# Performance work log

Hardware: AMD Instinct MI355X
Metric: run time of the kernel (lower is better)

## Reference

```python
import jax, jax.numpy as jnp
import numpy as np

EPS = 1e-5
NH = 4          # num_heads
DH = 128        # head_dim
ALPHA = 1.0 / float(np.sqrt(DH))


def _ln(x, w, b):
    m = x.mean(-1, keepdims=True)
    v = x.var(-1, keepdims=True)
    return (x - m) * jax.lax.rsqrt(v + EPS) * w + b


def setup_inputs() -> dict:
    key = jax.random.key(0)
    ks = jax.random.split(key, 8)
    D = 512                 # hidden_size
    U = 4 * NH * DH         # uvqk linear out = 2048
    B, S, H = 32, 256, 2048  # batch, new tokens/seq, history len/seq
    NT = B * S              # 8192 flattened jagged tokens
    layer_input = jax.random.normal(ks[0], (NT, D), dtype=jnp.float32)
    hist_k = jax.random.normal(ks[1], (B, H, NH, DH), dtype=jnp.float32) * 0.1
    hist_v = jax.random.normal(ks[2], (B, H, NH, DH), dtype=jnp.float32) * 0.1
    # torch init: uniform(-0.5, 0.5); scaled down for numerical sanity
    W_uvqk = (jax.random.uniform(ks[3], (D, U), dtype=jnp.float32) - 0.5) * 0.1
    b_uvqk = (jax.random.uniform(ks[4], (U,), dtype=jnp.float32) - 0.5) * 0.1
    ln_in_w = jnp.ones((D,), jnp.float32)
    ln_in_b = jnp.zeros((D,), jnp.float32)
    ln_out_w = jnp.ones((NH * DH,), jnp.float32)
    ln_out_b = jnp.zeros((NH * DH,), jnp.float32)
    W_proj = jax.random.normal(ks[5], (NH * DH, D), dtype=jnp.float32) * 0.05
    return {
        "layer_input": layer_input, "hist_k": hist_k, "hist_v": hist_v,
        "ln_in_w": ln_in_w, "ln_in_b": ln_in_b,
        "W_uvqk": W_uvqk, "b_uvqk": b_uvqk,
        "ln_out_w": ln_out_w, "ln_out_b": ln_out_b, "W_proj": W_proj,
    }


def reference(layer_input, hist_k, hist_v, ln_in_w, ln_in_b,
              W_uvqk, b_uvqk, ln_out_w, ln_out_b, W_proj):
    B, H, nh, dh = hist_k.shape
    NT, D = layer_input.shape
    S = NT // B
    dspl = nh * dh
    # ln -> linear+bias -> silu (fused u,v,q,k projection)
    x = _ln(layer_input, ln_in_w, ln_in_b)
    uvqk = jax.nn.silu(x @ W_uvqk + b_uvqk)
    u, v, q, k = jnp.split(uvqk, 4, axis=-1)   # order: user, value, query, key
    q = q.reshape(B, S, nh, dh)
    k = k.reshape(B, S, nh, dh)
    v = v.reshape(B, S, nh, dh)
    # paged KV-cache append == concat new k,v after history
    K = jnp.concatenate([hist_k, k], axis=1)   # [B, T, nh, dh], T = H+S
    V = jnp.concatenate([hist_v, v], axis=1)
    T = H + S
    # HSTU varlen attention: silu(alpha * q k^T) with causal delta-q mask,
    # query i sits at global position H+i and may attend to kv pos <= H+i
    scores = jnp.einsum('bsnd,btnd->bnst', q, K) * ALPHA
    mask = jnp.arange(T)[None, :] <= (H + jnp.arange(S))[:, None]  # [S, T]
    p = jnp.where(mask[None, None], jax.nn.silu(scores), 0.0)
    attn = jnp.einsum('bnst,btnd->bsnd', p, V).reshape(NT, dspl)
    # gated output LN, projection, residual
    parallel = u * _ln(attn, ln_out_w, ln_out_b)
    return parallel @ W_proj + layer_input
```

## Files before the change

kernel.cpp:

```cpp
#include <hip/hip_runtime.h>
#include <hip/hip_bf16.h>


typedef __attribute__((ext_vector_type(8))) short v8s;
typedef __attribute__((ext_vector_type(4))) float v4f;
typedef __attribute__((ext_vector_type(16))) float v16f;
typedef __attribute__((ext_vector_type(4))) unsigned short v4us;
typedef __attribute__((ext_vector_type(4))) unsigned int v4u;

#define D_HID 512
#define U_DIM 2048
#define NHEAD 4
#define DHEAD 128
#define BATCH 32
#define SEQ   256
#define HIST  2048
#define NTOK  8192
#define ALPHA_ 0.08838834764831845f
#define EPS_   1e-5f

__device__ __forceinline__ unsigned short f2bf(float f) {
  unsigned int u = __float_as_uint(f);
  u += 0x7FFFu + ((u >> 16) & 1u);
  return (unsigned short)(u >> 16);
}
__device__ __forceinline__ float bf2f(unsigned short s) {
  return __uint_as_float(((unsigned int)s) << 16);
}
__device__ __forceinline__ float siluf(float x) {
  return x * __builtin_amdgcn_rcpf(1.0f + __expf(-x));
}
__device__ __forceinline__ unsigned int cvtpk(float lo, float hi) {
  __hip_bfloat162 h = __float22bfloat162_rn(make_float2(lo, hi));
  union { __hip_bfloat162 h; unsigned int u; } cv; cv.h = h;
  return cv.u;
}

__global__ __launch_bounds__(256) void ln_in_kernel(
    const float* __restrict__ x, const float* __restrict__ w,
    const float* __restrict__ b, unsigned short* __restrict__ out)
{
  int wid = threadIdx.x >> 6, lane = threadIdx.x & 63;
  int row = blockIdx.x * 4 + wid;
  const float* xr = x + (size_t)row * D_HID + lane * 8;
  float4 a0 = *(const float4*)xr;
  float4 a1 = *(const float4*)(xr + 4);
  float v[8] = {a0.x, a0.y, a0.z, a0.w, a1.x, a1.y, a1.z, a1.w};
  float s = 0.f, s2 = 0.f;
#pragma unroll
  for (int j = 0; j < 8; ++j) { s += v[j]; s2 += v[j] * v[j]; }
#pragma unroll
  for (int m = 1; m < 64; m <<= 1) { s += __shfl_xor(s, m, 64); s2 += __shfl_xor(s2, m, 64); }
  float mean = s * (1.f / D_HID);
  float var  = s2 * (1.f / D_HID) - mean * mean;
  float rstd = rsqrtf(var + EPS_);
  const float* wp = w + lane * 8; const float* bp = b + lane * 8;
  float4 w0 = *(const float4*)wp, w1 = *(const float4*)(wp + 4);
  float4 b0 = *(const float4*)bp, b1 = *(const float4*)(bp + 4);
  float wv[8] = {w0.x, w0.y, w0.z, w0.w, w1.x, w1.y, w1.z, w1.w};
  float bv[8] = {b0.x, b0.y, b0.z, b0.w, b1.x, b1.y, b1.z, b1.w};
  v8s o;
#pragma unroll
  for (int j = 0; j < 8; ++j) o[j] = (short)f2bf((v[j] - mean) * rstd * wv[j] + bv[j]);
  *(v8s*)(out + (size_t)row * D_HID + lane * 8) = o;
}

__global__ __launch_bounds__(256) void gated_ln_kernel(
    const float* __restrict__ attn0, const float* __restrict__ attn1,
    const unsigned short* __restrict__ uvqk,
    const float* __restrict__ w, const float* __restrict__ b,
    unsigned short* __restrict__ par)
{
  int wid = threadIdx.x >> 6, lane = threadIdx.x & 63;
  int row = blockIdx.x * 4 + wid;
  size_t off = (size_t)row * D_HID + lane * 8;
  float4 x0 = *(const float4*)(attn0 + off), x1 = *(const float4*)(attn0 + off + 4);
  float4 y0 = *(const float4*)(attn1 + off), y1 = *(const float4*)(attn1 + off + 4);
  float v[8] = {x0.x + y0.x, x0.y + y0.y, x0.z + y0.z, x0.w + y0.w,
                x1.x + y1.x, x1.y + y1.y, x1.z + y1.z, x1.w + y1.w};
  float s = 0.f, s2 = 0.f;
#pragma unroll
  for (int j = 0; j < 8; ++j) { s += v[j]; s2 += v[j] * v[j]; }
#pragma unroll
  for (int m = 1; m < 64; m <<= 1) { s += __shfl_xor(s, m, 64); s2 += __shfl_xor(s2, m, 64); }
  float mean = s * (1.f / D_HID);
  float var  = s2 * (1.f / D_HID) - mean * mean;
  float rstd = rsqrtf(var + EPS_);
  const float* wp = w + lane * 8; const float* bp = b + lane * 8;
  float4 w0 = *(const float4*)wp, w1 = *(const float4*)(wp + 4);
  float4 b0 = *(const float4*)bp, b1 = *(const float4*)(bp + 4);
  float wv[8] = {w0.x, w0.y, w0.z, w0.w, w1.x, w1.y, w1.z, w1.w};
  float bv[8] = {b0.x, b0.y, b0.z, b0.w, b1.x, b1.y, b1.z, b1.w};
  v8s uv = *(const v8s*)(uvqk + (size_t)row * U_DIM + lane * 8);
  v8s o;
#pragma unroll
  for (int j = 0; j < 8; ++j) {
    float u = bf2f((unsigned short)uv[j]);
    o[j] = (short)f2bf(u * ((v[j] - mean) * rstd * wv[j] + bv[j]));
  }
  *(v8s*)(par + (size_t)row * D_HID + lane * 8) = o;
}

__global__ __launch_bounds__(256) void transpose_w_kernel(
    const float* __restrict__ in, unsigned short* __restrict__ out, int R, int C)
{
  __shared__ float tile[32][33];
  int c0 = blockIdx.x * 32, r0 = blockIdx.y * 32;
  int tr = threadIdx.x >> 3;
  int tc = (threadIdx.x & 7) * 4;
  float4 vv = *(const float4*)(in + (size_t)(r0 + tr) * C + c0 + tc);
  tile[tr][tc + 0] = vv.x; tile[tr][tc + 1] = vv.y;
  tile[tr][tc + 2] = vv.z; tile[tr][tc + 3] = vv.w;
  __syncthreads();
  v4us o;
#pragma unroll
  for (int j = 0; j < 4; ++j) o[j] = f2bf(tile[tc + j][tr]);
  *(v4us*)(out + (size_t)(c0 + tr) * R + r0 + tc) = o;
}

template <int EPI>
__global__ __launch_bounds__(256) void gemm_kernel(
    const unsigned short* __restrict__ A, const unsigned short* __restrict__ Bt,
    int K, int N,
    const float* __restrict__ bias, const float* __restrict__ resid,
    unsigned short* __restrict__ outb, float* __restrict__ outf)
{
  __shared__ unsigned short Al[128 * 64];
  __shared__ unsigned short Bl[128 * 64];
  int m0 = blockIdx.x * 128, n0 = blockIdx.y * 128;
  int tid = threadIdx.x, lane = tid & 63, wid = tid >> 6;
  int wr = wid >> 1, wc = wid & 1;
  int lr = lane & 15, lg = lane >> 4;
  int rkey = (lr & 7) << 3;

  v4f acc[4][4];
#pragma unroll
  for (int i = 0; i < 4; ++i)
#pragma unroll
    for (int j = 0; j < 4; ++j) acc[i][j] = (v4f){0.f, 0.f, 0.f, 0.f};

  int srow = tid >> 3;
  int scol = ((tid & 7) * 8) ^ ((srow & 7) << 3);
  const unsigned short* gA = A  + (size_t)(m0 + srow) * K + scol;
  const unsigned short* gB = Bt + (size_t)(n0 + srow) * K + scol;

  for (int k0 = 0; k0 < K; k0 += 64) {
#pragma unroll
    for (int c = 0; c < 4; ++c) {
      __builtin_amdgcn_global_load_lds(
          (const __attribute__((address_space(1))) unsigned int*)(gA + (size_t)(c * 32) * K + k0),
          (__attribute__((address_space(3))) unsigned int*)&Al[c * 2048 + wid * 512], 16, 0, 0);
      __builtin_amdgcn_global_load_lds(
          (const __attribute__((address_space(1))) unsigned int*)(gB + (size_t)(c * 32) * K + k0),
          (__attribute__((address_space(3))) unsigned int*)&Bl[c * 2048 + wid * 512], 16, 0, 0);
    }
    asm volatile("s_waitcnt vmcnt(0)" ::: "memory");
    __syncthreads();
#pragma unroll
    for (int kk = 0; kk < 2; ++kk) {
      v8s af[4], bf[4];
#pragma unroll
      for (int mt = 0; mt < 4; ++mt)
        af[mt] = *(const v8s*)&Al[(wr * 64 + mt * 16 + lr) * 64 + ((kk * 32 + lg * 8) ^ rkey)];
#pragma unroll
      for (int nt = 0; nt < 4; ++nt)
        bf[nt] = *(const v8s*)&Bl[(wc * 64 + nt * 16 + lr) * 64 + ((kk * 32 + lg * 8) ^ rkey)];
#pragma unroll
      for (int mt = 0; mt < 4; ++mt)
#pragma unroll
        for (int nt = 0; nt < 4; ++nt)
          acc[mt][nt] = __builtin_amdgcn_mfma_f32_16x16x32_bf16(af[mt], bf[nt], acc[mt][nt], 0, 0, 0);
    }
    __syncthreads();
  }

#pragma unroll
  for (int nt = 0; nt < 4; ++nt) {
    int col = n0 + wc * 64 + nt * 16 + lr;
    float bi = 0.f;
    if constexpr (EPI == 0) bi = bias[col];
#pragma unroll
    for (int mt = 0; mt < 4; ++mt) {
      int row0 = m0 + wr * 64 + mt * 16 + lg * 4;
#pragma unroll
      for (int r = 0; r < 4; ++r) {
        float xv = acc[mt][nt][r];
        if constexpr (EPI == 0) {
          float rv = siluf(xv + bi);
          if ((unsigned)(col - 2 * D_HID) < (unsigned)D_HID) rv *= ALPHA_;
          outb[(size_t)(row0 + r) * N + col] = f2bf(rv);
        } else {
          outf[(size_t)(row0 + r) * N + col] = xv + resid[(size_t)(row0 + r) * N + col];
        }
      }
    }
  }
}

__global__ __launch_bounds__(512, 2) void attn_kernel(
    const float* __restrict__ histK, const float* __restrict__ histV,
    const unsigned short* __restrict__ uvqk, float* __restrict__ attn_out)
{
  __shared__ __align__(16) unsigned short Kl[2 * 64 * 128];
  __shared__ __align__(16) unsigned short Vt[2 * 128 * 64];

  int bid = blockIdx.x;
  int q   = bid >> 7;
  int b   = (bid >> 2) & 31;
  int n   = bid & 3;
  int tbase0 = q * 1152;
  const int NT = 18;

  int tid = threadIdx.x, lane = tid & 63, w = tid >> 6;
  int l5 = lane & 31;
  int hi = lane >> 5;
  int hi8 = hi * 8;
  int sq = w * 32 + l5;

  v8s qf[8];
  {
    const unsigned short* qp = uvqk + (size_t)(b * SEQ + sq) * U_DIM
                               + 2 * D_HID + n * DHEAD + hi8;
#pragma unroll
    for (int ks = 0; ks < 8; ++ks) qf[ks] = *(const v8s*)(qp + ks * 16);
  }

  v16f oacc[4];
#pragma unroll
  for (int i = 0; i < 4; ++i)
#pragma unroll
    for (int r = 0; r < 16; ++r) oacc[i][r] = 0.f;

  int m     = tid & 15;
  int std0  = m * 8;
  int strow = tid >> 4;

  const float* kbase = histK + (((size_t)b * HIST) * NHEAD + n) * DHEAD + std0;
  const float* vbase = histV + (((size_t)b * HIST) * NHEAD + n) * DHEAD + std0;
  const unsigned short* nkbase = uvqk + (size_t)(b * SEQ) * U_DIM + 3 * D_HID + n * DHEAD + std0;
  const unsigned short* nvbase = uvqk + (size_t)(b * SEQ) * U_DIM + 1 * D_HID + n * DHEAD + std0;

  float4 hx[2][4];
  v8s    nx[2][2];
  int isnew_r = 0;

  auto stage_load = [&](int kt) {
    int tb = tbase0 + kt * 64;
    if (tb < HIST) {
      isnew_r = 0;
#pragma unroll
      for (int p = 0; p < 2; ++p) {
        unsigned off = ((unsigned)(tb + 2 * strow + p)) << 9;
        hx[p][0] = *(const float4*)(kbase + off);
        hx[p][1] = *(const float4*)(kbase + off + 4);
        hx[p][2] = *(const float4*)(vbase + off);
        hx[p][3] = *(const float4*)(vbase + off + 4);
      }
    } else {
      isnew_r = 1;
#pragma unroll
      for (int p = 0; p < 2; ++p) {
        unsigned off = ((unsigned)(tb - HIST + 2 * strow + p)) << 11;
        nx[p][0] = *(const v8s*)(nkbase + off);
        nx[p][1] = *(const v8s*)(nvbase + off);
      }
    }
  };

  auto stage_store = [&](int buf) {
    unsigned short* Kb = &Kl[buf * 8192];
    unsigned short* Vb = &Vt[buf * 8192];
    int t0 = 2 * strow;
    if (!isnew_r) {
#pragma unroll
      for (int p = 0; p < 2; ++p) {
        int t = t0 + p;
        v4u kp;
        kp[0] = cvtpk(hx[p][0].x, hx[p][0].y);
        kp[1] = cvtpk(hx[p][0].z, hx[p][0].w);
        kp[2] = cvtpk(hx[p][1].x, hx[p][1].y);
        kp[3] = cvtpk(hx[p][1].z, hx[p][1].w);
        *(v4u*)&Kb[t * 128 + (std0 ^ ((t & 7) << 3))] = kp;
      }
      float v0[8] = {hx[0][2].x, hx[0][2].y, hx[0][2].z, hx[0][2].w,
                     hx[0][3].x, hx[0][3].y, hx[0][3].z, hx[0][3].w};
      float v1[8] = {hx[1][2].x, hx[1][2].y, hx[1][2].z, hx[1][2].w,
                     hx[1][3].x, hx[1][3].y, hx[1][3].z, hx[1][3].w};
#pragma unroll
      for (int j = 0; j < 8; ++j) {
        int d = std0 + j;
        int col = t0 ^ ((((d >> 3) ^ d) & 7) << 3);
        *(unsigned int*)&Vb[d * 64 + col] = cvtpk(v0[j], v1[j]);
      }
    } else {
#pragma unroll
      for (int p = 0; p < 2; ++p) {
        int t = t0 + p;
        *(v8s*)&Kb[t * 128 + (std0 ^ ((t & 7) << 3))] = nx[p][0];
      }
#pragma unroll
      for (int j = 0; j < 8; ++j) {
        int d = std0 + j;
        int col = t0 ^ ((((d >> 3) ^ d) & 7) << 3);
        unsigned int pk = (unsigned int)(unsigned short)nx[0][1][j]
                        | ((unsigned int)(unsigned short)nx[1][1][j] << 16);
        *(unsigned int*)&Vb[d * 64 + col] = pk;
      }
    }
  };

  stage_load(0);
  stage_store(0);
  stage_load(1);
  __syncthreads();

  for (int kt = 0; kt < NT; ++kt) {
    int cur = kt & 1;
    if (kt + 1 < NT) stage_store(cur ^ 1);
    if (kt + 2 < NT) stage_load(kt + 2);

    int tb = tbase0 + kt * 64;
    bool masked = (tb >= HIST);
    const unsigned short* Kb = &Kl[cur * 8192];
    const unsigned short* Vb = &Vt[cur * 8192];

    __builtin_amdgcn_s_setprio(1);

    v8s pb[4];
    {
      v16f sa0, sa1;
#pragma unroll
      for (int r = 0; r < 16; ++r) { sa0[r] = 0.f; sa1[r] = 0.f; }
      int kx = (l5 & 7) << 3;
      int krow = l5 * 128;
#pragma unroll
      for (int ks = 0; ks < 8; ++ks) {
        int off = (ks * 16 + hi8) ^ kx;
        v8s kf0 = *(const v8s*)&Kb[krow + off];
        v8s kf1 = *(const v8s*)&Kb[krow + 4096 + off];
        sa0 = __builtin_amdgcn_mfma_f32_32x32x16_bf16(kf0, qf[ks], sa0, 0, 0, 0);
        sa1 = __builtin_amdgcn_mfma_f32_32x32x16_bf16(kf1, qf[ks], sa1, 0, 0, 0);
      }
#pragma unroll
      for (int tt = 0; tt < 2; ++tt) {
        v16f sa = tt ? sa1 : sa0;
        unsigned e[8];
        if (masked) {
          int thr = sq - (tb - HIST) - tt * 32 - 4 * hi;
#pragma unroll
          for (int i = 0; i < 8; ++i) {
            int r0 = 2 * i, r1 = 2 * i + 1;
            int tl0 = (r0 & 3) + 8 * (r0 >> 2);
            int tl1 = (r1 & 3) + 8 * (r1 >> 2);
            float p0 = (tl0 <= thr) ? siluf(sa[r0]) : 0.f;
            float p1 = (tl1 <= thr) ? siluf(sa[r1]) : 0.f;
            e[i] = cvtpk(p0, p1);
          }
        } else {
#pragma unroll
          for (int i = 0; i < 8; ++i) e[i] = cvtpk(siluf(sa[2 * i]), siluf(sa[2 * i + 1]));
        }
#pragma unroll
        for (int h = 0; h < 2; ++h) {
          unsigned a0 = e[h * 4 + 0], a1 = e[h * 4 + 1];
          unsigned b0 = e[h * 4 + 2], b1 = e[h * 4 + 3];
          unsigned sa0u = (unsigned)__shfl_xor((int)a0, 32, 64);
          unsigned sa1u = (unsigned)__shfl_xor((int)a1, 32, 64);
          unsigned sb0u = (unsigned)__shfl_xor((int)b0, 32, 64);
          unsigned sb1u = (unsigned)__shfl_xor((int)b1, 32, 64);
          union { unsigned u[4]; v8s s; } U;
          U.u[0] = hi ? sb0u : a0;
          U.u[1] = hi ? sb1u : a1;
          U.u[2] = hi ? b0 : sa0u;
          U.u[3] = hi ? b1 : sa1u;
          pb[tt * 2 + h] = U.s;
        }
      }
    }

#pragma unroll
    for (int ks = 0; ks < 4; ++ks) {
#pragma unroll
      for (int dt4 = 0; dt4 < 4; ++dt4) {
        int d = dt4 * 32 + l5;
        int col = (ks * 16 + hi8) ^ ((((d >> 3) ^ d) & 7) << 3);
        v8s vf = *(const v8s*)&Vb[d * 64 + col];
        oacc[dt4] = __builtin_amdgcn_mfma_f32_32x32x16_bf16(vf, pb[ks], oacc[dt4], 0, 0, 0);
      }
    }
    __builtin_amdgcn_s_setprio(0);

    if (kt + 1 < NT) __syncthreads();
  }

  {
    float* op = attn_out + (size_t)q * ((size_t)NTOK * D_HID)
              + (size_t)(b * SEQ + sq) * D_HID + n * DHEAD + 4 * hi;
#pragma unroll
    for (int dt4 = 0; dt4 < 4; ++dt4) {
#pragma unroll
      for (int g = 0; g < 4; ++g) {
        float4 o4 = make_float4(oacc[dt4][4 * g + 0], oacc[dt4][4 * g + 1],
                                oacc[dt4][4 * g + 2], oacc[dt4][4 * g + 3]);
        *(float4*)(op + dt4 * 32 + 8 * g) = o4;
      }
    }
  }
}

extern "C" void kernel_launch(void* const* d_in, const int* in_sizes, int n_in,
                              void* d_out, int out_size, void* d_ws, size_t ws_size,
                              hipStream_t stream)
{
  (void)in_sizes; (void)n_in; (void)out_size; (void)ws_size;

  const float* layer_input = (const float*)d_in[0];
  const float* hist_k   = (const float*)d_in[1];
  const float* hist_v   = (const float*)d_in[2];
  const float* ln_in_w  = (const float*)d_in[3];
  const float* ln_in_b  = (const float*)d_in[4];
  const float* W_uvqk   = (const float*)d_in[5];
  const float* b_uvqk   = (const float*)d_in[6];
  const float* ln_out_w = (const float*)d_in[7];
  const float* ln_out_b = (const float*)d_in[8];
  const float* W_proj   = (const float*)d_in[9];
  float* out = (float*)d_out;

  char* ws = (char*)d_ws;
  unsigned short* uvqk    = (unsigned short*)(ws);
  float*          attn0   = (float*)         (ws + (32u << 20));
  float*          attn1   = (float*)         (ws + (48u << 20));
  unsigned short* x_bf    = (unsigned short*)(ws + (48u << 20));
  unsigned short* par     = (unsigned short*)(ws + (64u << 20));
  unsigned short* wt_uvqk = (unsigned short*)(ws + (72u << 20));
  unsigned short* wt_proj = (unsigned short*)(ws + (74u << 20));

  ln_in_kernel<<<dim3(2048), dim3(256), 0, stream>>>(layer_input, ln_in_w, ln_in_b, x_bf);
  transpose_w_kernel<<<dim3(64, 16), dim3(256), 0, stream>>>(W_uvqk, wt_uvqk, 512, 2048);
  transpose_w_kernel<<<dim3(16, 16), dim3(256), 0, stream>>>(W_proj, wt_proj, 512, 512);
  gemm_kernel<0><<<dim3(64, 16), dim3(256), 0, stream>>>(x_bf, wt_uvqk, 512, 2048,
                                                         b_uvqk, nullptr, uvqk, nullptr);
  attn_kernel<<<dim3(256), dim3(512), 0, stream>>>(hist_k, hist_v, uvqk, attn0);
  gated_ln_kernel<<<dim3(2048), dim3(256), 0, stream>>>(attn0, attn1, uvqk, ln_out_w, ln_out_b, par);
  gemm_kernel<1><<<dim3(64, 4), dim3(256), 0, stream>>>(par, wt_proj, 512, 512,
                                                        nullptr, layer_input, nullptr, out);
}
```

Measured before the change: 157.5 us.

## Split attention queries across two 256-thread blocks, skip masked tail tiles, split staging

Each attention block now covers half of the 256 queries with 256 threads, so the grid doubles to 512 blocks. Blocks in the second KV half stop early once past the causal limit of their query half, skipping fully masked new-token tiles. The K/V tile staging is split into two 32-row halves placed around the QK and PV MFMA phases to spread global loads across the loop. The aim is better occupancy and load balance plus less wasted masked work, at the cost of each block reloading the full K/V stream for fewer queries.

```diff
diff --git a/kernel.cpp b/kernel.cpp
--- a/kernel.cpp
+++ b/kernel.cpp
@@ -197,7 +197,7 @@
   }
 }
 
-__global__ __launch_bounds__(512, 2) void attn_kernel(
+__global__ __launch_bounds__(256, 2) void attn_kernel(
     const float* __restrict__ histK, const float* __restrict__ histV,
     const unsigned short* __restrict__ uvqk, float* __restrict__ attn_out)
 {
@@ -205,17 +205,22 @@
   __shared__ __align__(16) unsigned short Vt[2 * 128 * 64];
 
   int bid = blockIdx.x;
-  int q   = bid >> 7;
+  int th  = bid >> 8;
+  int qh  = (bid >> 7) & 1;
   int b   = (bid >> 2) & 31;
   int n   = bid & 3;
-  int tbase0 = q * 1152;
-  const int NT = 18;
+  int tbase0 = th * 1152;
+  int NT = 18;
+  if (th == 1) {
+    int nt2 = (HIST + qh * 128 + 128 - tbase0 + 63) >> 6;
+    if (nt2 < NT) NT = nt2;
+  }
 
   int tid = threadIdx.x, lane = tid & 63, w = tid >> 6;
   int l5 = lane & 31;
   int hi = lane >> 5;
   int hi8 = hi * 8;
-  int sq = w * 32 + l5;
+  int sq = qh * 128 + w * 32 + l5;
 
   v8s qf[8];
   {
@@ -244,8 +249,8 @@
   v8s    nx[2][2];
   int isnew_r = 0;
 
-  auto stage_load = [&](int kt) {
-    int tb = tbase0 + kt * 64;
+  auto stage_load = [&](int kt, int h) {
+    int tb = tbase0 + kt * 64 + h * 32;
     if (tb < HIST) {
       isnew_r = 0;
 #pragma unroll
@@ -267,10 +272,10 @@
     }
   };
 
-  auto stage_store = [&](int buf) {
+  auto stage_store = [&](int buf, int h) {
     unsigned short* Kb = &Kl[buf * 8192];
     unsigned short* Vb = &Vt[buf * 8192];
-    int t0 = 2 * strow;
+    int t0 = h * 32 + 2 * strow;
     if (!isnew_r) {
 #pragma unroll
       for (int p = 0; p < 2; ++p) {
@@ -309,15 +314,14 @@
     }
   };
 
-  stage_load(0);
-  stage_store(0);
-  stage_load(1);
+  stage_load(0, 0); stage_store(0, 0);
+  stage_load(0, 1); stage_store(0, 1);
+  stage_load(1, 0);
   __syncthreads();
 
   for (int kt = 0; kt < NT; ++kt) {
     int cur = kt & 1;
-    if (kt + 1 < NT) stage_store(cur ^ 1);
-    if (kt + 2 < NT) stage_load(kt + 2);
+    if (kt + 1 < NT) { stage_store(cur ^ 1, 0); stage_load(kt + 1, 1); }
 
     int tb = tbase0 + kt * 64;
     bool masked = (tb >= HIST);
@@ -325,7 +329,6 @@
     const unsigned short* Vb = &Vt[cur * 8192];
 
     __builtin_amdgcn_s_setprio(1);
-
     v8s pb[4];
     {
       v16f sa0, sa1;
@@ -377,7 +380,12 @@
         }
       }
     }
-
+    __builtin_amdgcn_s_setprio(0);
+
+    if (kt + 1 < NT) stage_store(cur ^ 1, 1);
+    if (kt + 2 < NT) stage_load(kt + 2, 0);
+
+    __builtin_amdgcn_s_setprio(1);
 #pragma unroll
     for (int ks = 0; ks < 4; ++ks) {
 #pragma unroll
@@ -394,7 +402,7 @@
   }
 
   {
-    float* op = attn_out + (size_t)q * ((size_t)NTOK * D_HID)
+    float* op = attn_out + (size_t)th * ((size_t)NTOK * D_HID)
               + (size_t)(b * SEQ + sq) * D_HID + n * DHEAD + 4 * hi;
 #pragma unroll
     for (int dt4 = 0; dt4 < 4; ++dt4) {
@@ -440,7 +448,7 @@
   transpose_w_kernel<<<dim3(16, 16), dim3(256), 0, stream>>>(W_proj, wt_proj, 512, 512);
   gemm_kernel<0><<<dim3(64, 16), dim3(256), 0, stream>>>(x_bf, wt_uvqk, 512, 2048,
                                                          b_uvqk, nullptr, uvqk, nullptr);
-  attn_kernel<<<dim3(256), dim3(512), 0, stream>>>(hist_k, hist_v, uvqk, attn0);
+  attn_kernel<<<dim3(512), dim3(256), 0, stream>>>(hist_k, hist_v, uvqk, attn0);
   gated_ln_kernel<<<dim3(2048), dim3(256), 0, stream>>>(attn0, attn1, uvqk, ln_out_w, ln_out_b, par);
   gemm_kernel<1><<<dim3(64, 4), dim3(256), 0, stream>>>(par, wt_proj, 512, 512,
                                                         nullptr, layer_input, nullptr, out);
```

Measured after the change: 164.1 us. 1.04x slower.

## Double-buffer GEMM LDS tiles and reuse staging registers in attention

Applied to the files above, without the earlier changes.

The GEMM kernel now keeps two LDS buffers for the A and B tiles and prefetches the next K-tile with global_load_lds while MFMAs run on the current one. This lets global-to-LDS loads overlap with compute and needs only one barrier per iteration. In the attention kernel, new-token K/V loads reuse the float4 history staging registers instead of separate v8s registers to lower register pressure, and the P-packing loop becomes a lambda. Doubled LDS use in the GEMM may reduce occupancy.

```diff
diff --git a/kernel.cpp b/kernel.cpp
--- a/kernel.cpp
+++ b/kernel.cpp
@@ -125,8 +125,8 @@
     const float* __restrict__ bias, const float* __restrict__ resid,
     unsigned short* __restrict__ outb, float* __restrict__ outf)
 {
-  __shared__ unsigned short Al[128 * 64];
-  __shared__ unsigned short Bl[128 * 64];
+  __shared__ unsigned short Al[2][128 * 64];
+  __shared__ unsigned short Bl[2][128 * 64];
   int m0 = blockIdx.x * 128, n0 = blockIdx.y * 128;
   int tid = threadIdx.x, lane = tid & 63, wid = tid >> 6;
   int wr = wid >> 1, wc = wid & 1;
@@ -144,34 +144,45 @@
   const unsigned short* gA = A  + (size_t)(m0 + srow) * K + scol;
   const unsigned short* gB = Bt + (size_t)(n0 + srow) * K + scol;
 
-  for (int k0 = 0; k0 < K; k0 += 64) {
+  auto STAGE = [&](int buf, int k0) {
 #pragma unroll
     for (int c = 0; c < 4; ++c) {
       __builtin_amdgcn_global_load_lds(
           (const __attribute__((address_space(1))) unsigned int*)(gA + (size_t)(c * 32) * K + k0),
-          (__attribute__((address_space(3))) unsigned int*)&Al[c * 2048 + wid * 512], 16, 0, 0);
+          (__attribute__((address_space(3))) unsigned int*)&Al[buf][c * 2048 + wid * 512], 16, 0, 0);
       __builtin_amdgcn_global_load_lds(
           (const __attribute__((address_space(1))) unsigned int*)(gB + (size_t)(c * 32) * K + k0),
-          (__attribute__((address_space(3))) unsigned int*)&Bl[c * 2048 + wid * 512], 16, 0, 0);
-    }
-    asm volatile("s_waitcnt vmcnt(0)" ::: "memory");
-    __syncthreads();
+          (__attribute__((address_space(3))) unsigned int*)&Bl[buf][c * 2048 + wid * 512], 16, 0, 0);
+    }
+  };
+
+  const int NTk = K >> 6;
+  STAGE(0, 0);
+  asm volatile("s_waitcnt vmcnt(0)" ::: "memory");
+  __syncthreads();
+
+  for (int t = 0; t < NTk; ++t) {
+    int cur = t & 1;
+    if (t + 1 < NTk) STAGE(cur ^ 1, (t + 1) * 64);
 #pragma unroll
     for (int kk = 0; kk < 2; ++kk) {
       v8s af[4], bf[4];
 #pragma unroll
       for (int mt = 0; mt < 4; ++mt)
-        af[mt] = *(const v8s*)&Al[(wr * 64 + mt * 16 + lr) * 64 + ((kk * 32 + lg * 8) ^ rkey)];
+        af[mt] = *(const v8s*)&Al[cur][(wr * 64 + mt * 16 + lr) * 64 + ((kk * 32 + lg * 8) ^ rkey)];
 #pragma unroll
       for (int nt = 0; nt < 4; ++nt)
-        bf[nt] = *(const v8s*)&Bl[(wc * 64 + nt * 16 + lr) * 64 + ((kk * 32 + lg * 8) ^ rkey)];
+        bf[nt] = *(const v8s*)&Bl[cur][(wc * 64 + nt * 16 + lr) * 64 + ((kk * 32 + lg * 8) ^ rkey)];
 #pragma unroll
       for (int mt = 0; mt < 4; ++mt)
 #pragma unroll
         for (int nt = 0; nt < 4; ++nt)
           acc[mt][nt] = __builtin_amdgcn_mfma_f32_16x16x32_bf16(af[mt], bf[nt], acc[mt][nt], 0, 0, 0);
     }
-    __syncthreads();
+    if (t + 1 < NTk) {
+      asm volatile("s_waitcnt vmcnt(0)" ::: "memory");
+      __syncthreads();
+    }
   }
 
 #pragma unroll
@@ -241,7 +252,6 @@
   const unsigned short* nvbase = uvqk + (size_t)(b * SEQ) * U_DIM + 1 * D_HID + n * DHEAD + std0;
 
   float4 hx[2][4];
-  v8s    nx[2][2];
   int isnew_r = 0;
 
   auto stage_load = [&](int kt) {
@@ -261,8 +271,8 @@
 #pragma unroll
       for (int p = 0; p < 2; ++p) {
         unsigned off = ((unsigned)(tb - HIST + 2 * strow + p)) << 11;
-        nx[p][0] = *(const v8s*)(nkbase + off);
-        nx[p][1] = *(const v8s*)(nvbase + off);
+        hx[p][0] = *(const float4*)(const void*)(nkbase + off);
+        hx[p][2] = *(const float4*)(const void*)(nvbase + off);
       }
     }
   };
@@ -293,17 +303,20 @@
         *(unsigned int*)&Vb[d * 64 + col] = cvtpk(v0[j], v1[j]);
       }
     } else {
+      union { float4 f; v8s s; } ck0, ck1, cv0, cv1;
+      ck0.f = hx[0][0]; ck1.f = hx[1][0];
+      cv0.f = hx[0][2]; cv1.f = hx[1][2];
 #pragma unroll
       for (int p = 0; p < 2; ++p) {
         int t = t0 + p;
-        *(v8s*)&Kb[t * 128 + (std0 ^ ((t & 7) << 3))] = nx[p][0];
+        *(v8s*)&Kb[t * 128 + (std0 ^ ((t & 7) << 3))] = p ? ck1.s : ck0.s;
       }
 #pragma unroll
       for (int j = 0; j < 8; ++j) {
         int d = std0 + j;
         int col = t0 ^ ((((d >> 3) ^ d) & 7) << 3);
-        unsigned int pk = (unsigned int)(unsigned short)nx[0][1][j]
-                        | ((unsigned int)(unsigned short)nx[1][1][j] << 16);
+        unsigned int pk = (unsigned int)(unsigned short)cv0.s[j]
+                        | ((unsigned int)(unsigned short)cv1.s[j] << 16);
         *(unsigned int*)&Vb[d * 64 + col] = pk;
       }
     }
@@ -341,9 +354,7 @@
         sa0 = __builtin_amdgcn_mfma_f32_32x32x16_bf16(kf0, qf[ks], sa0, 0, 0, 0);
         sa1 = __builtin_amdgcn_mfma_f32_32x32x16_bf16(kf1, qf[ks], sa1, 0, 0, 0);
       }
-#pragma unroll
-      for (int tt = 0; tt < 2; ++tt) {
-        v16f sa = tt ? sa1 : sa0;
+      auto packP = [&](const v16f& sa, int tt) {
         unsigned e[8];
         if (masked) {
           int thr = sq - (tb - HIST) - tt * 32 - 4 * hi;
@@ -364,18 +375,20 @@
         for (int h = 0; h < 2; ++h) {
           unsigned a0 = e[h * 4 + 0], a1 = e[h * 4 + 1];
           unsigned b0 = e[h * 4 + 2], b1 = e[h * 4 + 3];
-          unsigned sa0u = (unsigned)__shfl_xor((int)a0, 32, 64);
-          unsigned sa1u = (unsigned)__shfl_xor((int)a1, 32, 64);
-          unsigned sb0u = (unsigned)__shfl_xor((int)b0, 32, 64);
-          unsigned sb1u = (unsigned)__shfl_xor((int)b1, 32, 64);
+          unsigned x0 = (unsigned)__shfl_xor((int)a0, 32, 64);
+          unsigned x1 = (unsigned)__shfl_xor((int)a1, 32, 64);
+          unsigned x2 = (unsigned)__shfl_xor((int)b0, 32, 64);
+          unsigned x3 = (unsigned)__shfl_xor((int)b1, 32, 64);
           union { unsigned u[4]; v8s s; } U;
-          U.u[0] = hi ? sb0u : a0;
-          U.u[1] = hi ? sb1u : a1;
-          U.u[2] = hi ? b0 : sa0u;
-          U.u[3] = hi ? b1 : sa1u;
+          U.u[0] = hi ? x2 : a0;
+          U.u[1] = hi ? x3 : a1;
+          U.u[2] = hi ? b0 : x0;
+          U.u[3] = hi ? b1 : x1;
           pb[tt * 2 + h] = U.s;
         }
-      }
+      };
+      packP(sa0, 0);
+      packP(sa1, 1);
     }
 
 #pragma unroll
```

Measured after the change: 223.6 us. 42.0% more time.
